# Optimization experiments

Hardware: AMD Instinct MI355X
Metric: run time of the kernel (lower is better)

## Reference

```python
import jax, jax.numpy as jnp
import numpy as np

WH, WW = 8, 8
N = WH * WW
DIM = 128
NUM_HEADS = 4
HEAD_DIM = DIM // NUM_HEADS
SCALE = HEAD_DIM ** -0.5


def _relative_position_index():
    coords = np.stack(np.meshgrid(np.arange(WH), np.arange(WW), indexing='ij'))  # (2, Wh, Ww)
    flat = coords.reshape(2, -1)  # (2, N)
    rel = flat[:, :, None] - flat[:, None, :]  # (2, N, N)
    rel = rel.transpose(1, 2, 0)  # (N, N, 2)
    rel[:, :, 0] += WH - 1
    rel[:, :, 1] += WW - 1
    rel[:, :, 0] *= 2 * WW - 1
    return rel.sum(-1)  # (N, N) int

REL_IDX = _relative_position_index()


def setup_inputs() -> dict:
    key = jax.random.key(0)
    ks = jax.random.split(key, 7)
    B_ = 4096
    nW = 64
    table_size = (2 * WH - 1) * (2 * WW - 1)  # 225
    return {
        'x': jax.random.normal(ks[0], (B_, N, DIM), dtype=jnp.float32),
        'mask': jax.random.normal(ks[1], (nW, N, N), dtype=jnp.float32),
        'qkv_w': jax.random.normal(ks[2], (3 * DIM, DIM), dtype=jnp.float32) * 0.02,
        'qkv_b': jnp.zeros((3 * DIM,), dtype=jnp.float32),
        'proj_w': jax.random.normal(ks[3], (DIM, DIM), dtype=jnp.float32) * 0.02,
        'proj_b': jnp.zeros((DIM,), dtype=jnp.float32),
        'bias_table': jax.random.normal(ks[4], (table_size, NUM_HEADS), dtype=jnp.float32) * 0.02,
    }


def reference(x, mask, qkv_w, qkv_b, proj_w, proj_b, bias_table):
    B_, n, C = x.shape
    nW = mask.shape[0]
    qkv = x @ qkv_w.T + qkv_b  # (B_, N, 3C)
    qkv = qkv.reshape(B_, n, 3, NUM_HEADS, HEAD_DIM)
    q = qkv[:, :, 0] * SCALE  # (B_, N, H, hd)
    k = qkv[:, :, 1]
    v = qkv[:, :, 2]
    attn = jnp.einsum('bihd,bjhd->bhij', q, k)  # (B_, H, N, N)
    rel_bias = bias_table[REL_IDX.reshape(-1)].reshape(n, n, NUM_HEADS)
    attn = attn + rel_bias.transpose(2, 0, 1)[None]  # broadcast over B_
    attn = attn.reshape(B_ // nW, nW, NUM_HEADS, n, n) + mask[None, :, None]
    attn = attn.reshape(B_, NUM_HEADS, n, n)
    attn = jax.nn.softmax(attn, axis=-1)
    out = jnp.einsum('bhij,bjhd->bihd', attn, v).reshape(B_, n, C)
    return out @ proj_w.T + proj_b
```

## Files before the change

### kernel.cpp

```cpp
#include <hip/hip_runtime.h>


typedef __bf16 bf16x8 __attribute__((ext_vector_type(8)));
typedef float f32x16 __attribute__((ext_vector_type(16)));

#define MFMA32(a, b, c) __builtin_amdgcn_mfma_f32_32x32x16_bf16(a, b, c, 0, 0, 0)
#define ATT_SCALE 0.17677669529663687f

__device__ __forceinline__ unsigned short f2bf(float f) {
  union { float fv; unsigned int u; } cv; cv.fv = f;
  unsigned int r = cv.u + 0x7FFFu + ((cv.u >> 16) & 1u);
  return (unsigned short)(r >> 16);
}

__device__ __forceinline__ unsigned pk2(float lo, float hi) {
  union { __bf16 h[2]; unsigned u; } t;
  t.h[0] = (__bf16)lo; t.h[1] = (__bf16)hi;
  return t.u;
}

__device__ __forceinline__ void pairw(float l0, float l1, float h0, float h1,
                                      int hl, unsigned &wlo, unsigned &whi) {
  unsigned lo = pk2(l0, l1);
  unsigned hi = pk2(h0, h1);
  unsigned los = (unsigned)__shfl_xor((int)lo, 32);
  unsigned his = (unsigned)__shfl_xor((int)hi, 32);
  wlo = hl ? his : lo;
  whi = hl ? hi : los;
}

__device__ __forceinline__ bf16x8 frag8(float a0, float a1, float a2, float a3,
                                        float a4, float a5, float a6, float a7,
                                        int hl) {
  union { unsigned u[4]; bf16x8 v; } r;
  pairw(a0, a1, a4, a5, hl, r.u[0], r.u[2]);
  pairw(a2, a3, a6, a7, hl, r.u[1], r.u[3]);
  return r.v;
}

#define FRAG_LO(p) frag8(p[0], p[1], p[2], p[3], p[4], p[5], p[6], p[7], hl)
#define FRAG_HI(p) frag8(p[8], p[9], p[10], p[11], p[12], p[13], p[14], p[15], hl)

__global__ __launch_bounds__(256) void convert_weights(
    const float* __restrict__ qkv_w, const float* __restrict__ proj_w,
    unsigned short* __restrict__ wq, unsigned short* __restrict__ wp) {
  int t = blockIdx.x * 256 + threadIdx.x;
  if (t < 384 * 128) {
    float v = qkv_w[t];
    if (t < 128 * 128) v *= ATT_SCALE;
    wq[t] = f2bf(v);
  } else {
    wp[t - 384 * 128] = f2bf(proj_w[t - 384 * 128]);
  }
}

__global__ __launch_bounds__(256) void build_cb(
    const float* __restrict__ mask, const float* __restrict__ bias_table,
    float* __restrict__ cb) {
  int t = blockIdx.x * 256 + threadIdx.x;
  int ij = t & 4095;
  int h = (t >> 12) & 3;
  int w = t >> 14;
  int j = ij >> 6, i = ij & 63;
  int ridx = ((i >> 3) - (j >> 3) + 7) * 15 + ((i & 7) - (j & 7) + 7);
  cb[t] = bias_table[ridx * 4 + h] + mask[(w << 12) + (i << 6) + j];
}

__global__ __launch_bounds__(256, 4) void window_attn(
    const float* __restrict__ x, const float* __restrict__ qkv_b,
    const float* __restrict__ proj_b, const unsigned short* __restrict__ wq,
    const unsigned short* __restrict__ wp, const float* __restrict__ cbT,
    float* __restrict__ out, int nW) {
  __shared__ unsigned short Xb[64][136];
  __shared__ unsigned short Vt[4][32][72];

  const int tid = threadIdx.x;
  const int h = tid >> 6;
  const int lane = tid & 63;
  const int l31 = lane & 31;
  const int hl = lane >> 5;
  const int b = blockIdx.x;
  const int w = b % nW;

  const float* xb = x + (size_t)b * 8192;
  #pragma unroll
  for (int st = 0; st < 8; ++st) {
    int e = (st * 256 + tid) * 4;
    float4 v4 = *reinterpret_cast<const float4*>(xb + e);
    ushort4 o;
    o.x = f2bf(v4.x); o.y = f2bf(v4.y); o.z = f2bf(v4.z); o.w = f2bf(v4.w);
    *reinterpret_cast<ushort4*>(&Xb[e >> 7][e & 127]) = o;
  }
  __syncthreads();

  {
    f32x16 av0, av1;
    #pragma unroll
    for (int q = 0; q < 16; ++q) { av0[q] = 0.0f; av1[q] = 0.0f; }
    const unsigned short* wvp = wq + (size_t)(256 + h * 32 + l31) * 128 + hl * 8;
    #pragma unroll
    for (int kt = 0; kt < 8; ++kt) {
      bf16x8 aw = *reinterpret_cast<const bf16x8*>(wvp + kt * 16);
      bf16x8 b0 = *reinterpret_cast<const bf16x8*>(&Xb[l31][kt * 16 + hl * 8]);
      bf16x8 b1 = *reinterpret_cast<const bf16x8*>(&Xb[32 + l31][kt * 16 + hl * 8]);
      av0 = MFMA32(aw, b0, av0);
      av1 = MFMA32(aw, b1, av1);
    }
    #pragma unroll
    for (int r = 0; r < 16; ++r) {
      int dr = (r & 3) + 8 * (r >> 2) + 4 * hl;
      float bv = qkv_b[256 + h * 32 + dr];
      Vt[h][dr][l31]      = f2bf(av0[r] + bv);
      Vt[h][dr][32 + l31] = f2bf(av1[r] + bv);
    }
  }

  f32x16 aq[2], ak[2];
  #pragma unroll
  for (int t2 = 0; t2 < 2; ++t2)
    #pragma unroll
    for (int q = 0; q < 16; ++q) { aq[t2][q] = 0.0f; ak[t2][q] = 0.0f; }
  {
    const unsigned short* wqp = wq + (size_t)(h * 32 + l31) * 128 + hl * 8;
    const unsigned short* wkp = wq + (size_t)(128 + h * 32 + l31) * 128 + hl * 8;
    #pragma unroll
    for (int kt = 0; kt < 8; ++kt) {
      bf16x8 b0 = *reinterpret_cast<const bf16x8*>(&Xb[l31][kt * 16 + hl * 8]);
      bf16x8 b1 = *reinterpret_cast<const bf16x8*>(&Xb[32 + l31][kt * 16 + hl * 8]);
      bf16x8 awq = *reinterpret_cast<const bf16x8*>(wqp + kt * 16);
      bf16x8 awk = *reinterpret_cast<const bf16x8*>(wkp + kt * 16);
      aq[0] = MFMA32(awq, b0, aq[0]);
      aq[1] = MFMA32(awq, b1, aq[1]);
      ak[0] = MFMA32(awk, b0, ak[0]);
      ak[1] = MFMA32(awk, b1, ak[1]);
    }
  }
  __syncthreads();

  #pragma unroll
  for (int r = 0; r < 16; ++r) {
    int dr = (r & 3) + 8 * (r >> 2) + 4 * hl;
    float bq = qkv_b[h * 32 + dr] * ATT_SCALE;
    float bk = qkv_b[128 + h * 32 + dr];
    aq[0][r] += bq; aq[1][r] += bq;
    ak[0][r] += bk; ak[1][r] += bk;
  }

  bf16x8 qf[2][2], kf[2][2];
  #pragma unroll
  for (int t2 = 0; t2 < 2; ++t2) {
    qf[t2][0] = FRAG_LO(aq[t2]); qf[t2][1] = FRAG_HI(aq[t2]);
    kf[t2][0] = FRAG_LO(ak[t2]); kf[t2][1] = FRAG_HI(ak[t2]);
  }

  f32x16 sacc[2][2];
  #pragma unroll
  for (int mt = 0; mt < 2; ++mt)
    #pragma unroll
    for (int it = 0; it < 2; ++it) {
      #pragma unroll
      for (int q = 0; q < 16; ++q) sacc[mt][it][q] = 0.0f;
      sacc[mt][it] = MFMA32(kf[mt][0], qf[it][0], sacc[mt][it]);
      sacc[mt][it] = MFMA32(kf[mt][1], qf[it][1], sacc[mt][it]);
    }

  const float* cbp = cbT + (((size_t)w * 4 + h) << 12);
  float rinv[2];
  #pragma unroll
  for (int it = 0; it < 2; ++it) {
    #pragma unroll
    for (int mt = 0; mt < 2; ++mt)
      #pragma unroll
      for (int r = 0; r < 16; ++r) {
        int jr = (r & 3) + 8 * (r >> 2) + 4 * hl + 32 * mt;
        sacc[mt][it][r] += cbp[jr * 64 + 32 * it + l31];
      }
    float m = sacc[0][it][0];
    #pragma unroll
    for (int mt = 0; mt < 2; ++mt)
      #pragma unroll
      for (int r = 0; r < 16; ++r) m = fmaxf(m, sacc[mt][it][r]);
    m = fmaxf(m, __shfl_xor(m, 32));
    float sum = 0.0f;
    #pragma unroll
    for (int mt = 0; mt < 2; ++mt)
      #pragma unroll
      for (int r = 0; r < 16; ++r) {
        float e = __expf(sacc[mt][it][r] - m);
        sacc[mt][it][r] = e;
        sum += e;
      }
    sum += __shfl_xor(sum, 32);
    rinv[it] = __builtin_amdgcn_rcpf(sum);
  }

  bf16x8 pf0[4], pf1[4];
  pf0[0] = FRAG_LO(sacc[0][0]); pf0[1] = FRAG_HI(sacc[0][0]);
  pf0[2] = FRAG_LO(sacc[1][0]); pf0[3] = FRAG_HI(sacc[1][0]);
  pf1[0] = FRAG_LO(sacc[0][1]); pf1[1] = FRAG_HI(sacc[0][1]);
  pf1[2] = FRAG_LO(sacc[1][1]); pf1[3] = FRAG_HI(sacc[1][1]);

  f32x16 o0, o1;
  #pragma unroll
  for (int q = 0; q < 16; ++q) { o0[q] = 0.0f; o1[q] = 0.0f; }
  #pragma unroll
  for (int kt = 0; kt < 4; ++kt) {
    bf16x8 aV = *reinterpret_cast<const bf16x8*>(&Vt[h][l31][kt * 16 + hl * 8]);
    o0 = MFMA32(aV, pf0[kt], o0);
    o1 = MFMA32(aV, pf1[kt], o1);
  }
  #pragma unroll
  for (int r = 0; r < 16; ++r) {
    int dr = (r & 3) + 8 * (r >> 2) + 4 * hl;
    Xb[l31][h * 32 + dr]      = f2bf(o0[r] * rinv[0]);
    Xb[32 + l31][h * 32 + dr] = f2bf(o1[r] * rinv[1]);
  }
  __syncthreads();

  {
    const int c = h * 32 + l31;
    const float pb = proj_b[c];
    const unsigned short* wrow = wp + (size_t)c * 128 + hl * 8;
    bf16x8 bfr[8];
    #pragma unroll
    for (int kt = 0; kt < 8; ++kt)
      bfr[kt] = *reinterpret_cast<const bf16x8*>(wrow + kt * 16);
    float* ob = out + (size_t)b * 8192;
    #pragma unroll
    for (int mt = 0; mt < 2; ++mt) {
      f32x16 acc;
      #pragma unroll
      for (int q = 0; q < 16; ++q) acc[q] = 0.0f;
      #pragma unroll
      for (int kt = 0; kt < 8; ++kt) {
        bf16x8 a = *reinterpret_cast<const bf16x8*>(&Xb[mt * 32 + l31][kt * 16 + hl * 8]);
        acc = MFMA32(a, bfr[kt], acc);
      }
      #pragma unroll
      for (int r = 0; r < 16; ++r) {
        int row = (r & 3) + 8 * (r >> 2) + 4 * hl + mt * 32;
        ob[row * 128 + c] = acc[r] + pb;
      }
    }
  }
}

extern "C" void kernel_launch(void* const* d_in, const int* in_sizes, int n_in,
                              void* d_out, int out_size, void* d_ws, size_t ws_size,
                              hipStream_t stream) {
  const float* x          = (const float*)d_in[0];
  const float* mask       = (const float*)d_in[1];
  const float* qkv_w      = (const float*)d_in[2];
  const float* qkv_b      = (const float*)d_in[3];
  const float* proj_w     = (const float*)d_in[4];
  const float* proj_b     = (const float*)d_in[5];
  const float* bias_table = (const float*)d_in[6];
  const int B_ = in_sizes[0] / 8192;
  const int nW = in_sizes[1] / 4096;

  unsigned short* wq = (unsigned short*)d_ws;
  unsigned short* wp = wq + 384 * 128;
  float* cbuf = (float*)((char*)d_ws + 131072);

  convert_weights<<<(384 * 128 + 128 * 128) / 256, 256, 0, stream>>>(qkv_w, proj_w, wq, wp);
  build_cb<<<(nW * 4 * 4096) / 256, 256, 0, stream>>>(mask, bias_table, cbuf);
  window_attn<<<B_, 256, 0, stream>>>(x, qkv_b, proj_b, wq, wp, cbuf, (float*)d_out, nW);
}
```

Before: 366.4 us.

## Restructure attention per query tile to cut register pressure and lower occupancy bound

Moves the score, softmax and PV computation into a loop over the two query tiles, so only one tile's scores and output accumulator are live at a time. The combined bias/mask is loaded straight into the MFMA accumulator instead of being added afterwards, and the max/sum reductions are rewritten as trees. The launch bound drops from 4 to 3 waves per SIMD, giving the compiler more registers and aiming to avoid spills at the cost of lower occupancy.

```diff
diff --git a/kernel.cpp b/kernel.cpp
--- a/kernel.cpp
+++ b/kernel.cpp
@@ -66,7 +66,7 @@
   cb[t] = bias_table[ridx * 4 + h] + mask[(w << 12) + (i << 6) + j];
 }
 
-__global__ __launch_bounds__(256, 4) void window_attn(
+__global__ __launch_bounds__(256, 3) void window_attn(
     const float* __restrict__ x, const float* __restrict__ qkv_b,
     const float* __restrict__ proj_b, const unsigned short* __restrict__ wq,
     const unsigned short* __restrict__ wp, const float* __restrict__ cbT,
@@ -115,12 +115,13 @@
     }
   }
 
-  f32x16 aq[2], ak[2];
-  #pragma unroll
-  for (int t2 = 0; t2 < 2; ++t2)
-    #pragma unroll
-    for (int q = 0; q < 16; ++q) { aq[t2][q] = 0.0f; ak[t2][q] = 0.0f; }
+  bf16x8 qf[2][2], kf[2][2];
   {
+    f32x16 aq[2], ak[2];
+    #pragma unroll
+    for (int t2 = 0; t2 < 2; ++t2)
+      #pragma unroll
+      for (int q = 0; q < 16; ++q) { aq[t2][q] = 0.0f; ak[t2][q] = 0.0f; }
     const unsigned short* wqp = wq + (size_t)(h * 32 + l31) * 128 + hl * 8;
     const unsigned short* wkp = wq + (size_t)(128 + h * 32 + l31) * 128 + hl * 8;
     #pragma unroll
@@ -134,86 +135,83 @@
       ak[0] = MFMA32(awk, b0, ak[0]);
       ak[1] = MFMA32(awk, b1, ak[1]);
     }
-  }
-  __syncthreads();
-
-  #pragma unroll
-  for (int r = 0; r < 16; ++r) {
-    int dr = (r & 3) + 8 * (r >> 2) + 4 * hl;
-    float bq = qkv_b[h * 32 + dr] * ATT_SCALE;
-    float bk = qkv_b[128 + h * 32 + dr];
-    aq[0][r] += bq; aq[1][r] += bq;
-    ak[0][r] += bk; ak[1][r] += bk;
-  }
-
-  bf16x8 qf[2][2], kf[2][2];
-  #pragma unroll
-  for (int t2 = 0; t2 < 2; ++t2) {
-    qf[t2][0] = FRAG_LO(aq[t2]); qf[t2][1] = FRAG_HI(aq[t2]);
-    kf[t2][0] = FRAG_LO(ak[t2]); kf[t2][1] = FRAG_HI(ak[t2]);
-  }
-
-  f32x16 sacc[2][2];
-  #pragma unroll
-  for (int mt = 0; mt < 2; ++mt)
-    #pragma unroll
-    for (int it = 0; it < 2; ++it) {
-      #pragma unroll
-      for (int q = 0; q < 16; ++q) sacc[mt][it][q] = 0.0f;
-      sacc[mt][it] = MFMA32(kf[mt][0], qf[it][0], sacc[mt][it]);
-      sacc[mt][it] = MFMA32(kf[mt][1], qf[it][1], sacc[mt][it]);
-    }
+    __syncthreads();
+
+    #pragma unroll
+    for (int r = 0; r < 16; ++r) {
+      int dr = (r & 3) + 8 * (r >> 2) + 4 * hl;
+      float bq = qkv_b[h * 32 + dr] * ATT_SCALE;
+      float bk = qkv_b[128 + h * 32 + dr];
+      aq[0][r] += bq; aq[1][r] += bq;
+      ak[0][r] += bk; ak[1][r] += bk;
+    }
+
+    #pragma unroll
+    for (int t2 = 0; t2 < 2; ++t2) {
+      kf[t2][0] = FRAG_LO(ak[t2]); kf[t2][1] = FRAG_HI(ak[t2]);
+    }
+    #pragma unroll
+    for (int t2 = 0; t2 < 2; ++t2) {
+      qf[t2][0] = FRAG_LO(aq[t2]); qf[t2][1] = FRAG_HI(aq[t2]);
+    }
+  }
 
   const float* cbp = cbT + (((size_t)w * 4 + h) << 12);
-  float rinv[2];
   #pragma unroll
   for (int it = 0; it < 2; ++it) {
+    f32x16 s[2];
     #pragma unroll
     for (int mt = 0; mt < 2; ++mt)
       #pragma unroll
       for (int r = 0; r < 16; ++r) {
         int jr = (r & 3) + 8 * (r >> 2) + 4 * hl + 32 * mt;
-        sacc[mt][it][r] += cbp[jr * 64 + 32 * it + l31];
+        s[mt][r] = cbp[jr * 64 + 32 * it + l31];
       }
-    float m = sacc[0][it][0];
+    #pragma unroll
+    for (int mt = 0; mt < 2; ++mt) {
+      s[mt] = MFMA32(kf[mt][0], qf[it][0], s[mt]);
+      s[mt] = MFMA32(kf[mt][1], qf[it][1], s[mt]);
+    }
+
+    float mx[8];
+    #pragma unroll
+    for (int r = 0; r < 8; ++r)
+      mx[r] = fmaxf(fmaxf(s[0][r], s[0][r + 8]), fmaxf(s[1][r], s[1][r + 8]));
+    mx[0] = fmaxf(mx[0], mx[4]); mx[1] = fmaxf(mx[1], mx[5]);
+    mx[2] = fmaxf(mx[2], mx[6]); mx[3] = fmaxf(mx[3], mx[7]);
+    float m = fmaxf(fmaxf(mx[0], mx[1]), fmaxf(mx[2], mx[3]));
+    m = fmaxf(m, __shfl_xor(m, 32));
     #pragma unroll
     for (int mt = 0; mt < 2; ++mt)
       #pragma unroll
-      for (int r = 0; r < 16; ++r) m = fmaxf(m, sacc[mt][it][r]);
-    m = fmaxf(m, __shfl_xor(m, 32));
-    float sum = 0.0f;
-    #pragma unroll
-    for (int mt = 0; mt < 2; ++mt)
-      #pragma unroll
-      for (int r = 0; r < 16; ++r) {
-        float e = __expf(sacc[mt][it][r] - m);
-        sacc[mt][it][r] = e;
-        sum += e;
-      }
+      for (int r = 0; r < 16; ++r)
+        s[mt][r] = __expf(s[mt][r] - m);
+    float sm[8];
+    #pragma unroll
+    for (int r = 0; r < 8; ++r)
+      sm[r] = (s[0][r] + s[0][r + 8]) + (s[1][r] + s[1][r + 8]);
+    sm[0] += sm[4]; sm[1] += sm[5]; sm[2] += sm[6]; sm[3] += sm[7];
+    float sum = (sm[0] + sm[1]) + (sm[2] + sm[3]);
     sum += __shfl_xor(sum, 32);
-    rinv[it] = __builtin_amdgcn_rcpf(sum);
-  }
-
-  bf16x8 pf0[4], pf1[4];
-  pf0[0] = FRAG_LO(sacc[0][0]); pf0[1] = FRAG_HI(sacc[0][0]);
-  pf0[2] = FRAG_LO(sacc[1][0]); pf0[3] = FRAG_HI(sacc[1][0]);
-  pf1[0] = FRAG_LO(sacc[0][1]); pf1[1] = FRAG_HI(sacc[0][1]);
-  pf1[2] = FRAG_LO(sacc[1][1]); pf1[3] = FRAG_HI(sacc[1][1]);
-
-  f32x16 o0, o1;
-  #pragma unroll
-  for (int q = 0; q < 16; ++q) { o0[q] = 0.0f; o1[q] = 0.0f; }
-  #pragma unroll
-  for (int kt = 0; kt < 4; ++kt) {
-    bf16x8 aV = *reinterpret_cast<const bf16x8*>(&Vt[h][l31][kt * 16 + hl * 8]);
-    o0 = MFMA32(aV, pf0[kt], o0);
-    o1 = MFMA32(aV, pf1[kt], o1);
-  }
-  #pragma unroll
-  for (int r = 0; r < 16; ++r) {
-    int dr = (r & 3) + 8 * (r >> 2) + 4 * hl;
-    Xb[l31][h * 32 + dr]      = f2bf(o0[r] * rinv[0]);
-    Xb[32 + l31][h * 32 + dr] = f2bf(o1[r] * rinv[1]);
+    const float rinv = __builtin_amdgcn_rcpf(sum);
+
+    bf16x8 pf[4];
+    pf[0] = FRAG_LO(s[0]); pf[1] = FRAG_HI(s[0]);
+    pf[2] = FRAG_LO(s[1]); pf[3] = FRAG_HI(s[1]);
+
+    f32x16 o;
+    #pragma unroll
+    for (int q = 0; q < 16; ++q) o[q] = 0.0f;
+    #pragma unroll
+    for (int kt = 0; kt < 4; ++kt) {
+      bf16x8 aV = *reinterpret_cast<const bf16x8*>(&Vt[h][l31][kt * 16 + hl * 8]);
+      o = MFMA32(aV, pf[kt], o);
+    }
+    #pragma unroll
+    for (int r = 0; r < 16; ++r) {
+      int dr = (r & 3) + 8 * (r >> 2) + 4 * hl;
+      Xb[32 * it + l31][h * 32 + dr] = f2bf(o[r] * rinv);
+    }
   }
   __syncthreads();
 
```

Result: faster. 318.9 us (-13.0%).
